# Performance work log

Hardware: AMD Instinct MI355X
Metric: run time of the kernel (lower is better)

Reference implementation:

```python
import jax, jax.numpy as jnp
import numpy as np

# Dims: B=batch, C=n_car, N=n_node, E=embed_dim, H=n_heads
B, C, N, E = 64, 8, 512, 512
H = 8
CLIP = 10.0


def setup_inputs() -> dict:
    key = jax.random.key(0)
    ks = jax.random.split(key, 12)
    s = 1.0 / np.sqrt(E)
    mask = jax.random.bernoulli(ks[10], 0.3, (B, C, 1, N))
    mask = mask.at[..., 0].set(False)  # ensure at least one unmasked node per (b,c)
    return {
        "node_embeddings": jax.random.normal(ks[0], (B, N, E), jnp.float32),
        "graph_embedding": jax.random.normal(ks[1], (B, E), jnp.float32),
        "step_context": jax.random.normal(ks[2], (B, C, 1, E + 2), jnp.float32),
        "mask": mask,
        "Wk1": jax.random.normal(ks[3], (E, E), jnp.float32) * s,
        "Wv": jax.random.normal(ks[4], (E, E), jnp.float32) * s,
        "Wk2": jax.random.normal(ks[5], (E, E), jnp.float32) * s,
        "Wq_fixed": jax.random.normal(ks[6], (E, E), jnp.float32) * s,
        "Wout": jax.random.normal(ks[7], (E, E), jnp.float32) * s,
        "Wq_step": jax.random.normal(ks[8], (E, E + 2), jnp.float32) * s,
        "v": jax.random.uniform(ks[9], (E,), jnp.float32, -s, s),
    }


def reference(node_embeddings, graph_embedding, step_context, mask,
              Wk1, Wv, Wk2, Wq_fixed, Wout, Wq_step, v):
    dh = E // H
    neg = jnp.asarray(-1e9, node_embeddings.dtype)

    # compute_static: projections (torch Linear: x @ W.T). K/V/Q_fixed are
    # broadcast over the car dim instead of materialized via .repeat (same math).
    Q_fixed = (graph_embedding @ Wq_fixed.T)[:, None, None, :]  # [B,1,1,E]
    K1 = node_embeddings @ Wk1.T                                 # [B,N,E]
    V = node_embeddings @ Wv.T                                   # [B,N,E]
    K2 = node_embeddings @ Wk2.T                                 # [B,N,E]

    # compute_dynamic
    Q_step = step_context @ Wq_step.T                            # [B,C,1,E]
    Q1 = Q_fixed + Q_step                                        # [B,C,1,E]

    # MHA (need_W=False): split heads, masked scaled dot-product, merge heads.
    qh = Q1.reshape(B, C, H, dh)                                 # q-len 1 squeezed
    kh = K1.reshape(B, N, H, dh)
    vh = V.reshape(B, N, H, dh)
    scores = jnp.einsum('bchd,bnhd->bchn', qh, kh) * (1.0 / np.sqrt(dh))
    m = mask[:, :, 0, :][:, :, None, :]                          # [B,C,1,N]
    scores = jnp.where(m, neg, scores)
    attn = jax.nn.softmax(scores, axis=-1)
    heads = jnp.einsum('bchn,bnhd->bchd', attn, vh).reshape(B, C, E)
    Q3 = heads @ Wout.T                                          # [B,C,E] (Q2.squeeze(2))

    # Pointer logits (SHA): u = tanh(Q_fixed+Q_step) @ v, repeated over E,
    # dotted with K2 => u_scalar * sum_e K2, then tanh-clipped and masked.
    u_scalar = jnp.einsum('bcqe,e->bcq', jnp.tanh(Q1), v)        # [B,C,1]
    k2sum = K2.sum(-1)                                           # [B,N]
    raw = u_scalar * k2sum[:, None, :]                           # [B,C,N]
    logits = CLIP * jnp.tanh(raw * (1.0 / np.sqrt(E)))
    logits = jnp.where(mask[:, :, 0, :], neg, logits)
    logits = logits.reshape(B, C * N)                            # view(batch, -1)
    return logits, Q3
```

## Files before the change

### kernel.cpp

```cpp
#include <hip/hip_runtime.h>


typedef _Float16 f16x8 __attribute__((ext_vector_type(8)));
typedef float f32x4 __attribute__((ext_vector_type(4)));

__device__ __forceinline__ void async16(const void* g, void* l) {
  __builtin_amdgcn_global_load_lds(
      (const __attribute__((address_space(1))) unsigned int*)g,
      (__attribute__((address_space(3))) unsigned int*)l, 16, 0, 0);
}

__device__ __forceinline__ float fast_tanh(float x) {
  float ax = fabsf(x);
  float t = __expf(-2.f * ax);
  float r = (1.f - t) / (1.f + t);
  return copysignf(r, x);
}

__global__ __launch_bounds__(256) void prep_q1(
    const float* __restrict__ Wk1, const float* __restrict__ Wv,
    const float* __restrict__ Wk2, _Float16* __restrict__ W1h,
    _Float16* __restrict__ W2h, float* __restrict__ colsum,
    const float* __restrict__ ge, const float* __restrict__ sc,
    const float* __restrict__ Wqf, const float* __restrict__ Wqs,
    float* __restrict__ Q1) {
  const int bid = blockIdx.x;
  if (bid < 272) {
    if (bid < 16) {
      const int tx = threadIdx.x & 31, ty = threadIdx.x >> 5;
      const int col = bid * 32 + tx;
      float s = 0.f;
#pragma unroll 4
      for (int e = ty * 64; e < ty * 64 + 64; ++e) s += Wk2[e * 512 + col];
      __shared__ float red[8][32];
      red[ty][tx] = s;
      __syncthreads();
      if (ty == 0) {
        float t = 0.f;
#pragma unroll
        for (int g = 0; g < 8; ++g) t += red[g][tx];
        colsum[col] = t;
      }
    } else {
      const int cb = bid - 16;
      const float* src = (cb < 128) ? Wk1 : Wv;
      _Float16* dst = (cb < 128) ? W1h : W2h;
      const size_t off = (size_t)(cb & 127) * 2048 + threadIdx.x * 8;
      float4 a = *(const float4*)(src + off);
      float4 b = *(const float4*)(src + off + 4);
      union { _Float16 h[8]; uint4 u; } pk;
      pk.h[0] = (_Float16)a.x; pk.h[1] = (_Float16)a.y;
      pk.h[2] = (_Float16)a.z; pk.h[3] = (_Float16)a.w;
      pk.h[4] = (_Float16)b.x; pk.h[5] = (_Float16)b.y;
      pk.h[6] = (_Float16)b.z; pk.h[7] = (_Float16)b.w;
      *(uint4*)(dst + off) = pk.u;
    }
    return;
  }

  const int b2 = bid - 272;
  const int mb = b2 & 7, nb = (b2 >> 3) & 7, ks = b2 >> 6;
  const int tid = threadIdx.x;
  const int lane = tid & 63, wave = tid >> 6;
  const int wm = (wave >> 1) * 32, wn = (wave & 1) * 32;

  __shared__ __align__(16) _Float16 As[64][40];
  __shared__ __align__(16) _Float16 Ws[64][40];

  f32x4 acc[2][2] = {};
  const int qd = (lane >> 4) * 8, rr = lane & 15;

  for (int kt = 0; kt < 9; ++kt) {
    const int kb = ks * 288 + kt * 32;
#pragma unroll
    for (int f0 = 0; f0 < 2; ++f0) {
      int f = tid + f0 * 256;
      int r = f >> 3, c4 = (f & 7) * 4;
      int m = mb * 64 + r;
      int e = nb * 64 + r;
#pragma unroll
      for (int j = 0; j < 4; ++j) {
        int k = kb + c4 + j;
        float a = 0.f, w = 0.f;
        if (k < 512) {
          a = ge[(m >> 3) * 512 + k];
          w = Wqf[(size_t)e * 512 + k];
        } else if (k < 1026) {
          a = sc[(size_t)m * 514 + (k - 512)];
          w = Wqs[(size_t)e * 514 + (k - 512)];
        }
        As[r][c4 + j] = (_Float16)a;
        Ws[r][c4 + j] = (_Float16)w;
      }
    }
    __syncthreads();
    f16x8 af[2], bfr[2];
#pragma unroll
    for (int mi = 0; mi < 2; ++mi) af[mi] = *(const f16x8*)&As[wm + mi * 16 + rr][qd];
#pragma unroll
    for (int ni = 0; ni < 2; ++ni) bfr[ni] = *(const f16x8*)&Ws[wn + ni * 16 + rr][qd];
#pragma unroll
    for (int mi = 0; mi < 2; ++mi)
#pragma unroll
      for (int ni = 0; ni < 2; ++ni)
        acc[mi][ni] =
            __builtin_amdgcn_mfma_f32_16x16x32_f16(af[mi], bfr[ni], acc[mi][ni], 0, 0, 0);
    __syncthreads();
  }

  const int col = lane & 15, rq = (lane >> 4) * 4;
#pragma unroll
  for (int mi = 0; mi < 2; ++mi)
#pragma unroll
    for (int ni = 0; ni < 2; ++ni)
#pragma unroll
      for (int r = 0; r < 4; ++r) {
        int m = mb * 64 + wm + mi * 16 + rq + r;
        int e = nb * 64 + wn + ni * 16 + col;
        atomicAdd(&Q1[(size_t)m * 512 + e], acc[mi][ni][r]);
      }
}

__global__ __launch_bounds__(256, 2) void gemm_kv(
    const float* __restrict__ A, const _Float16* __restrict__ W1,
    const _Float16* __restrict__ W2, const float* __restrict__ colsum,
    _Float16* __restrict__ K1, _Float16* __restrict__ Vt,
    float* __restrict__ k2sum) {
  const int flat = (int)(blockIdx.y * 4 + blockIdx.x);
  const int work = (flat & 7) * 128 + (flat >> 3);
  const int nb = work & 3;
  const int mb = work >> 2;
  const int tid = threadIdx.x, lane = tid & 63, wave = tid >> 6;
  const int wm = (wave >> 1) * 64, wn = (wave & 1) * 64;
  const int row0 = mb * 128, col0 = nb * 128;
  const int b = mb >> 2;

  __shared__ __align__(16) _Float16 Ah[128 * 64];
  __shared__ __align__(16) _Float16 Wb[2][2][128 * 64];

  f32x4 acc1[4][4] = {}, acc2[4][4] = {};
  float k2p[4] = {0.f, 0.f, 0.f, 0.f};
  const int q = lane >> 4, rr = lane & 15;
  const int wlr = lane >> 3, wlc = lane & 7;
  const int cswz = wlc ^ wlr;

  const int ar0 = tid >> 3, ac = tid & 7;
  const float* aptr = A + (size_t)(row0 + ar0) * 512 + ac * 8;
  const int aslot = ac ^ (ar0 & 7);

  float4 areg[4][2];
  float4 cs0, cs1;

  auto issue_a = [&](int kt) {
#pragma unroll
    for (int j = 0; j < 4; ++j) {
      const float* gp = aptr + (size_t)j * 32 * 512 + kt * 64;
      areg[j][0] = *(const float4*)gp;
      areg[j][1] = *(const float4*)(gp + 4);
    }
    if (nb == 0) {
      const float* csp = colsum + kt * 64 + ac * 8;
      cs0 = *(const float4*)csp;
      cs1 = *(const float4*)(csp + 4);
    }
  };
  auto issue_w = [&](int kt, int buf) {
    const int kbase = kt * 64;
#pragma unroll
    for (int j = 0; j < 4; ++j) {
      int r = wave * 32 + j * 8 + wlr;
      int ldsrow = (wave * 32 + j * 8) * 64;
      size_t goff = (size_t)(col0 + r) * 512 + kbase + cswz * 8;
      async16(W1 + goff, &Wb[buf][0][ldsrow]);
      async16(W2 + goff, &Wb[buf][1][ldsrow]);
    }
  };
  auto write_a = [&](int kt) {
#pragma unroll
    for (int j = 0; j < 4; ++j) {
      union { _Float16 h[8]; uint4 u; } pk;
      float4 lo = areg[j][0], hi = areg[j][1];
      pk.h[0] = (_Float16)lo.x; pk.h[1] = (_Float16)lo.y;
      pk.h[2] = (_Float16)lo.z; pk.h[3] = (_Float16)lo.w;
      pk.h[4] = (_Float16)hi.x; pk.h[5] = (_Float16)hi.y;
      pk.h[6] = (_Float16)hi.z; pk.h[7] = (_Float16)hi.w;
      *(uint4*)&Ah[(ar0 + 32 * j) * 64 + aslot * 8] = pk.u;
    }
    if (nb == 0) {
#pragma unroll
      for (int j = 0; j < 4; ++j) {
        float4 lo = areg[j][0], hi = areg[j][1];
        k2p[j] += lo.x * cs0.x + lo.y * cs0.y + lo.z * cs0.z + lo.w * cs0.w +
                  hi.x * cs1.x + hi.y * cs1.y + hi.z * cs1.z + hi.w * cs1.w;
      }
    }
  };

  issue_a(0);
  issue_w(0, 0);
  write_a(0);
  __syncthreads();

  for (int kt = 0; kt < 8; ++kt) {
    const int p = kt & 1;
    if (kt < 7) {
      issue_a(kt + 1);
      issue_w(kt + 1, p ^ 1);
    }
#pragma unroll
    for (int k0 = 0; k0 < 64; k0 += 32) {
      const int cb = (k0 >> 3) + q;
      f16x8 af[4], b1[4], b2[4];
#pragma unroll
      for (int mi = 0; mi < 4; ++mi) {
        int ra = wm + mi * 16 + rr;
        af[mi] = *(const f16x8*)&Ah[ra * 64 + (cb ^ (ra & 7)) * 8];
      }
#pragma unroll
      for (int ni = 0; ni < 4; ++ni) {
        int rw = wn + ni * 16 + rr;
        int slot = cb ^ (rw & 7);
        b1[ni] = *(const f16x8*)&Wb[p][0][rw * 64 + slot * 8];
        b2[ni] = *(const f16x8*)&Wb[p][1][rw * 64 + slot * 8];
      }
      __builtin_amdgcn_s_setprio(1);
#pragma unroll
      for (int mi = 0; mi < 4; ++mi)
#pragma unroll
        for (int ni = 0; ni < 4; ++ni) {
          acc1[mi][ni] =
              __builtin_amdgcn_mfma_f32_16x16x32_f16(af[mi], b1[ni], acc1[mi][ni], 0, 0, 0);
          acc2[mi][ni] =
              __builtin_amdgcn_mfma_f32_16x16x32_f16(af[mi], b2[ni], acc2[mi][ni], 0, 0, 0);
        }
      __builtin_amdgcn_s_setprio(0);
    }
    if (kt < 7) {
      __syncthreads();
      write_a(kt + 1);
      __syncthreads();
    }
  }

  if (nb == 0) {
#pragma unroll
    for (int j = 0; j < 4; ++j) {
      float s = k2p[j];
      s += __shfl_xor(s, 1, 8);
      s += __shfl_xor(s, 2, 8);
      s += __shfl_xor(s, 4, 8);
      if (ac == 0) k2sum[row0 + ar0 + 32 * j] = s;
    }
  }

  const int col = lane & 15, rq = (lane >> 4) * 4;
#pragma unroll
  for (int mi = 0; mi < 4; ++mi)
#pragma unroll
    for (int ni = 0; ni < 4; ++ni)
#pragma unroll
      for (int r = 0; r < 4; ++r) {
        size_t m = row0 + wm + mi * 16 + rq + r;
        size_t e = col0 + wn + ni * 16 + col;
        K1[m * 512 + e] = (_Float16)acc1[mi][ni][r];
      }

  _Float16* Vts = &Wb[0][0][0];
#pragma unroll
  for (int mi = 0; mi < 4; ++mi)
#pragma unroll
    for (int ni = 0; ni < 4; ++ni) {
      int n0 = wm + mi * 16 + rq;
      int el = wn + ni * 16 + col;
      int cn = n0 >> 3, half = (n0 >> 2) & 1;
      int slot = cn ^ (el & 7);
      union { _Float16 h[4]; unsigned long long u; } pk;
#pragma unroll
      for (int r = 0; r < 4; ++r) pk.h[r] = (_Float16)acc2[mi][ni][r];
      *(unsigned long long*)&Vts[el * 128 + slot * 8 + half * 4] = pk.u;
    }
  __syncthreads();
  const int nbase = row0 & 511;
#pragma unroll
  for (int i = 0; i < 8; ++i) {
    int f = tid + i * 256;
    int el = f >> 4, c16 = f & 15;
    int slot = c16 ^ (el & 7);
    uint4 val = *(const uint4*)&Vts[el * 128 + slot * 8];
    *(uint4*)(Vt + (size_t)b * 262144 + (size_t)(col0 + el) * 512 + nbase + c16 * 8) = val;
  }
}

__global__ __launch_bounds__(256) void attn_kernel(
    const float* __restrict__ Q1, const _Float16* __restrict__ K1,
    const _Float16* __restrict__ Vt, const int* __restrict__ mask,
    float* __restrict__ heads) {
  const int bid = blockIdx.x;
  const int b = bid >> 3, h = bid & 7;
  const int tid = threadIdx.x, wave = tid >> 6, lane = tid & 63;
  const int q = lane >> 4, cl = lane & 15;

  __shared__ __align__(16) _Float16 kt[256 * 64];
  __shared__ __align__(16) _Float16 P[16][520];
  __shared__ float red[4][8];

  f16x8 af[2];
  {
    const float* qp = Q1 + (size_t)(b * 8 + (cl & 7)) * 512 + h * 64 + q * 8;
#pragma unroll
    for (int s = 0; s < 2; ++s) {
      float4 l0 = *(const float4*)(qp + s * 32);
      float4 l1 = *(const float4*)(qp + s * 32 + 4);
      af[s][0] = (_Float16)l0.x; af[s][1] = (_Float16)l0.y;
      af[s][2] = (_Float16)l0.z; af[s][3] = (_Float16)l0.w;
      af[s][4] = (_Float16)l1.x; af[s][5] = (_Float16)l1.y;
      af[s][6] = (_Float16)l1.z; af[s][7] = (_Float16)l1.w;
    }
  }

  f32x4 acc[8] = {};
  const _Float16* Kb = K1 + (size_t)b * 262144 + h * 64;
  for (int h2 = 0; h2 < 2; ++h2) {
#pragma unroll
    for (int j = 0; j < 8; ++j) {
      int r = wave * 64 + j * 8 + (lane >> 3);
      int cg = (lane & 7) ^ (r & 7);
      async16(Kb + (size_t)(h2 * 256 + r) * 512 + cg * 8, &kt[(wave * 64 + j * 8) * 64]);
    }
    __syncthreads();
    __builtin_amdgcn_s_setprio(1);
#pragma unroll
    for (int tt = 0; tt < 4; ++tt) {
      int rn = wave * 64 + tt * 16 + cl;
#pragma unroll
      for (int s = 0; s < 2; ++s) {
        int slot = (s * 4 + q) ^ (cl & 7);
        f16x8 bf = *(const f16x8*)&kt[rn * 64 + slot * 8];
        acc[h2 * 4 + tt] =
            __builtin_amdgcn_mfma_f32_16x16x32_f16(af[s], bf, acc[h2 * 4 + tt], 0, 0, 0);
      }
    }
    __builtin_amdgcn_s_setprio(0);
    __syncthreads();
  }

  const _Float16* Vb = Vt + (size_t)b * 262144 + (size_t)h * 64 * 512;
#pragma unroll
  for (int j = 0; j < 8; ++j) {
    int r = wave * 16 + j * 2 + (lane >> 5);
    int cg = (lane & 31) ^ (r & 7);
    async16(Vb + (size_t)r * 512 + cg * 8, &kt[(wave * 16 + j * 2) * 256]);
  }

  float gmax[4], rsum[4];
  if (q < 2) {
    float mx[4] = {-3e38f, -3e38f, -3e38f, -3e38f};
#pragma unroll
    for (int t = 0; t < 8; ++t) {
      int n = (t >> 2) * 256 + wave * 64 + (t & 3) * 16 + cl;
#pragma unroll
      for (int r = 0; r < 4; ++r) {
        int c = q * 4 + r;
        float x = mask[(size_t)(b * 8 + c) * 512 + n] ? -1e9f : acc[t][r] * 0.125f;
        acc[t][r] = x;
        mx[r] = fmaxf(mx[r], x);
      }
    }
#pragma unroll
    for (int off = 1; off < 16; off <<= 1)
#pragma unroll
      for (int r = 0; r < 4; ++r) mx[r] = fmaxf(mx[r], __shfl_xor(mx[r], off, 64));
    if (cl == 0)
#pragma unroll
      for (int r = 0; r < 4; ++r) red[wave][q * 4 + r] = mx[r];
  }
  __syncthreads();
  if (q < 2) {
#pragma unroll
    for (int r = 0; r < 4; ++r) {
      int c = q * 4 + r;
      gmax[r] = fmaxf(fmaxf(red[0][c], red[1][c]), fmaxf(red[2][c], red[3][c]));
    }
  }
  __syncthreads();
  if (q < 2) {
#pragma unroll
    for (int r = 0; r < 4; ++r) rsum[r] = 0.f;
#pragma unroll
    for (int t = 0; t < 8; ++t) {
      int n = (t >> 2) * 256 + wave * 64 + (t & 3) * 16 + cl;
#pragma unroll
      for (int r = 0; r < 4; ++r) {
        float e = __expf(acc[t][r] - gmax[r]);
        rsum[r] += e;
        P[q * 4 + r][n] = (_Float16)e;
      }
    }
#pragma unroll
    for (int off = 1; off < 16; off <<= 1)
#pragma unroll
      for (int r = 0; r < 4; ++r) rsum[r] += __shfl_xor(rsum[r], off, 64);
    if (cl == 0)
#pragma unroll
      for (int r = 0; r < 4; ++r) red[wave][q * 4 + r] = rsum[r];
  }
  __syncthreads();

  f32x4 pacc = {};
  const int rn = wave * 16 + cl;
  __builtin_amdgcn_s_setprio(1);
#pragma unroll
  for (int sl = 0; sl < 8; ++sl) {
    int slot = (sl * 4 + q) ^ (cl & 7);
    f16x8 bf = *(const f16x8*)&kt[rn * 256 + slot * 8];
    f16x8 pa = *(const f16x8*)&P[cl][sl * 32 + q * 8];
    pacc = __builtin_amdgcn_mfma_f32_16x16x32_f16(pa, bf, pacc, 0, 0, 0);
  }
  __builtin_amdgcn_s_setprio(0);
  __syncthreads();
#pragma unroll
  for (int j = 0; j < 8; ++j) {
    int r = wave * 16 + j * 2 + (lane >> 5);
    int cg = (lane & 31) ^ (r & 7);
    async16(Vb + (size_t)r * 512 + 256 + cg * 8, &kt[(wave * 16 + j * 2) * 256]);
  }
  __syncthreads();
  __builtin_amdgcn_s_setprio(1);
#pragma unroll
  for (int sl = 0; sl < 8; ++sl) {
    int slot = (sl * 4 + q) ^ (cl & 7);
    f16x8 bf = *(const f16x8*)&kt[rn * 256 + slot * 8];
    f16x8 pa = *(const f16x8*)&P[cl][256 + sl * 32 + q * 8];
    pacc = __builtin_amdgcn_mfma_f32_16x16x32_f16(pa, bf, pacc, 0, 0, 0);
  }
  __builtin_amdgcn_s_setprio(0);

  if (q < 2) {
#pragma unroll
    for (int r = 0; r < 4; ++r) {
      int c = q * 4 + r;
      float inv = 1.f / (red[0][c] + red[1][c] + red[2][c] + red[3][c]);
      heads[(size_t)(b * 8 + c) * 512 + h * 64 + wave * 16 + cl] = pacc[r] * inv;
    }
  }
}

__global__ __launch_bounds__(256) void out_logits(
    const float* __restrict__ A, const float* __restrict__ W,
    float* __restrict__ C, const float* __restrict__ Q1,
    const float* __restrict__ v, const float* __restrict__ k2s,
    const int* __restrict__ mask, float* __restrict__ out) {
  const int bid = blockIdx.x;
  if (bid < 64) {
    const int mb = bid & 7, nb = bid >> 3;
    const int tid = threadIdx.x;
    const int lane = tid & 63, wave = tid >> 6;
    const int wm = (wave >> 1) * 32, wn = (wave & 1) * 32;

    __shared__ __align__(16) _Float16 As[64][40];
    __shared__ __align__(16) _Float16 Ws[64][40];

    f32x4 acc[2][2] = {};
    const int qd = (lane >> 4) * 8, rr = lane & 15;

    for (int kt = 0; kt < 16; ++kt) {
      const int kb = kt * 32;
#pragma unroll
      for (int f0 = 0; f0 < 2; ++f0) {
        int f = tid + f0 * 256;
        int r = f >> 3, c4 = (f & 7) * 4;
        float4 a = *(const float4*)(A + (size_t)(mb * 64 + r) * 512 + kb + c4);
        float4 w = *(const float4*)(W + (size_t)(nb * 64 + r) * 512 + kb + c4);
        As[r][c4 + 0] = (_Float16)a.x; As[r][c4 + 1] = (_Float16)a.y;
        As[r][c4 + 2] = (_Float16)a.z; As[r][c4 + 3] = (_Float16)a.w;
        Ws[r][c4 + 0] = (_Float16)w.x; Ws[r][c4 + 1] = (_Float16)w.y;
        Ws[r][c4 + 2] = (_Float16)w.z; Ws[r][c4 + 3] = (_Float16)w.w;
      }
      __syncthreads();
      f16x8 af[2], bfr[2];
#pragma unroll
      for (int mi = 0; mi < 2; ++mi) af[mi] = *(const f16x8*)&As[wm + mi * 16 + rr][qd];
#pragma unroll
      for (int ni = 0; ni < 2; ++ni) bfr[ni] = *(const f16x8*)&Ws[wn + ni * 16 + rr][qd];
#pragma unroll
      for (int mi = 0; mi < 2; ++mi)
#pragma unroll
        for (int ni = 0; ni < 2; ++ni)
          acc[mi][ni] =
              __builtin_amdgcn_mfma_f32_16x16x32_f16(af[mi], bfr[ni], acc[mi][ni], 0, 0, 0);
      __syncthreads();
    }

    const int col = lane & 15, rq = (lane >> 4) * 4;
#pragma unroll
    for (int mi = 0; mi < 2; ++mi)
#pragma unroll
      for (int ni = 0; ni < 2; ++ni)
#pragma unroll
        for (int r = 0; r < 4; ++r) {
          int m = mb * 64 + wm + mi * 16 + rq + r;
          int e = nb * 64 + wn + ni * 16 + col;
          C[(size_t)m * 512 + e] = acc[mi][ni][r];
        }
    return;
  }

  const int bc = bid - 64;
  const int b = bc >> 3;
  const int tid = threadIdx.x;
  const int wave = tid >> 6, lane = tid & 63;

  float p = fast_tanh(Q1[(size_t)bc * 512 + tid]) * v[tid] +
            fast_tanh(Q1[(size_t)bc * 512 + tid + 256]) * v[tid + 256];
#pragma unroll
  for (int off = 32; off; off >>= 1) p += __shfl_down(p, off, 64);
  __shared__ float red[4];
  __shared__ float su;
  if (lane == 0) red[wave] = p;
  __syncthreads();
  if (tid == 0) su = red[0] + red[1] + red[2] + red[3];
  __syncthreads();
  const float u = su;

#pragma unroll
  for (int i = 0; i < 2; ++i) {
    int n = tid + i * 256;
    int idx = bc * 512 + n;
    out[idx] = mask[idx] ? -1e9f
                         : 10.f * fast_tanh(u * k2s[b * 512 + n] * 0.04419417382415922f);
  }
}

extern "C" void kernel_launch(void* const* d_in, const int* in_sizes, int n_in,
                              void* d_out, int out_size, void* d_ws, size_t ws_size,
                              hipStream_t stream) {
  const float* ne = (const float*)d_in[0];
  const float* ge = (const float*)d_in[1];
  const float* sc = (const float*)d_in[2];
  const int* mask = (const int*)d_in[3];
  const float* Wk1 = (const float*)d_in[4];
  const float* Wv = (const float*)d_in[5];
  const float* Wk2 = (const float*)d_in[6];
  const float* Wqf = (const float*)d_in[7];
  const float* Wout = (const float*)d_in[8];
  const float* Wqs = (const float*)d_in[9];
  const float* v = (const float*)d_in[10];

  float* logits = (float*)d_out;
  float* q3 = (float*)d_out + 262144;

  char* ws = (char*)d_ws;
  _Float16* K1 = (_Float16*)(ws + 0);
  _Float16* Vt = (_Float16*)(ws + 33554432);
  float* Q1 = (float*)(ws + 67108864);
  float* heads = (float*)(ws + 68157440);
  float* k2sum = (float*)(ws + 69206016);
  float* colsum = (float*)(ws + 69337088);
  _Float16* W1h = (_Float16*)(ws + 69339136);
  _Float16* W2h = (_Float16*)(ws + 69863424);

  hipMemsetAsync(Q1, 0, 1048576, stream);
  prep_q1<<<528, 256, 0, stream>>>(Wk1, Wv, Wk2, W1h, W2h, colsum,
                                   ge, sc, Wqf, Wqs, Q1);
  gemm_kv<<<dim3(4, 256), 256, 0, stream>>>(ne, W1h, W2h, colsum, K1, Vt, k2sum);
  attn_kernel<<<512, 256, 0, stream>>>(Q1, K1, Vt, mask, heads);
  out_logits<<<576, 256, 0, stream>>>(heads, Wout, q3, Q1, v, k2sum, mask, logits);
}
```

Baseline: 209.6 us.

## Double-buffer K/V tiles in attention kernel and split P into halves

The attention kernel now uses two LDS buffers, so the second K half and both V halves are prefetched while the QK MFMAs and softmax run. Before, each load had to wait on the previous compute. P is shrunk to a half-width buffer that is refilled between the two PV passes, and the second half of the exp computation is deferred until after the first PV pass. This adds LDS usage (two 32KB buffers), which may lower occupancy, and changes the barrier schedule.

```diff
diff --git a/kernel.cpp b/kernel.cpp
--- a/kernel.cpp
+++ b/kernel.cpp
@@ -300,8 +300,8 @@
   const int tid = threadIdx.x, wave = tid >> 6, lane = tid & 63;
   const int q = lane >> 4, cl = lane & 15;
 
-  __shared__ __align__(16) _Float16 kt[256 * 64];
-  __shared__ __align__(16) _Float16 P[16][520];
+  __shared__ __align__(16) _Float16 buf[2][256 * 64];
+  __shared__ __align__(16) _Float16 P[16][264];
   __shared__ float red[4][8];
 
   f16x8 af[2];
@@ -318,16 +318,28 @@
     }
   }
 
-  f32x4 acc[8] = {};
   const _Float16* Kb = K1 + (size_t)b * 262144 + h * 64;
-  for (int h2 = 0; h2 < 2; ++h2) {
+  const _Float16* Vb = Vt + (size_t)b * 262144 + (size_t)h * 64 * 512;
+
+  auto stage_K = [&](_Float16* dst, int rbase) {
 #pragma unroll
     for (int j = 0; j < 8; ++j) {
       int r = wave * 64 + j * 8 + (lane >> 3);
       int cg = (lane & 7) ^ (r & 7);
-      async16(Kb + (size_t)(h2 * 256 + r) * 512 + cg * 8, &kt[(wave * 64 + j * 8) * 64]);
-    }
-    __syncthreads();
+      async16(Kb + (size_t)(rbase + r) * 512 + cg * 8, &dst[(wave * 64 + j * 8) * 64]);
+    }
+  };
+  auto stage_V = [&](_Float16* dst, int noff) {
+#pragma unroll
+    for (int j = 0; j < 8; ++j) {
+      int r = wave * 16 + j * 2 + (lane >> 5);
+      int cg = (lane & 31) ^ (r & 7);
+      async16(Vb + (size_t)r * 512 + noff + cg * 8, &dst[(wave * 16 + j * 2) * 256]);
+    }
+  };
+
+  f32x4 acc[8] = {};
+  auto qk_half = [&](const _Float16* src, int h2) {
     __builtin_amdgcn_s_setprio(1);
 #pragma unroll
     for (int tt = 0; tt < 4; ++tt) {
@@ -335,24 +347,25 @@
 #pragma unroll
       for (int s = 0; s < 2; ++s) {
         int slot = (s * 4 + q) ^ (cl & 7);
-        f16x8 bf = *(const f16x8*)&kt[rn * 64 + slot * 8];
+        f16x8 bf = *(const f16x8*)&src[rn * 64 + slot * 8];
         acc[h2 * 4 + tt] =
             __builtin_amdgcn_mfma_f32_16x16x32_f16(af[s], bf, acc[h2 * 4 + tt], 0, 0, 0);
       }
     }
     __builtin_amdgcn_s_setprio(0);
-    __syncthreads();
-  }
-
-  const _Float16* Vb = Vt + (size_t)b * 262144 + (size_t)h * 64 * 512;
-#pragma unroll
-  for (int j = 0; j < 8; ++j) {
-    int r = wave * 16 + j * 2 + (lane >> 5);
-    int cg = (lane & 31) ^ (r & 7);
-    async16(Vb + (size_t)r * 512 + cg * 8, &kt[(wave * 16 + j * 2) * 256]);
-  }
-
-  float gmax[4], rsum[4];
+  };
+
+  stage_K(buf[0], 0);
+  __syncthreads();
+  stage_K(buf[1], 256);
+  qk_half(buf[0], 0);
+  __syncthreads();
+  stage_V(buf[0], 0);
+  qk_half(buf[1], 1);
+  __syncthreads();
+  stage_V(buf[1], 256);
+
+  float gmax[4], rsum[4] = {0.f, 0.f, 0.f, 0.f};
   if (q < 2) {
     float mx[4] = {-3e38f, -3e38f, -3e38f, -3e38f};
 #pragma unroll
@@ -381,28 +394,16 @@
       int c = q * 4 + r;
       gmax[r] = fmaxf(fmaxf(red[0][c], red[1][c]), fmaxf(red[2][c], red[3][c]));
     }
-  }
-  __syncthreads();
-  if (q < 2) {
-#pragma unroll
-    for (int r = 0; r < 4; ++r) rsum[r] = 0.f;
-#pragma unroll
-    for (int t = 0; t < 8; ++t) {
-      int n = (t >> 2) * 256 + wave * 64 + (t & 3) * 16 + cl;
+#pragma unroll
+    for (int t = 0; t < 4; ++t) {
+      int np = wave * 64 + (t & 3) * 16 + cl;
 #pragma unroll
       for (int r = 0; r < 4; ++r) {
         float e = __expf(acc[t][r] - gmax[r]);
         rsum[r] += e;
-        P[q * 4 + r][n] = (_Float16)e;
-      }
-    }
-#pragma unroll
-    for (int off = 1; off < 16; off <<= 1)
-#pragma unroll
-      for (int r = 0; r < 4; ++r) rsum[r] += __shfl_xor(rsum[r], off, 64);
-    if (cl == 0)
-#pragma unroll
-      for (int r = 0; r < 4; ++r) red[wave][q * 4 + r] = rsum[r];
+        P[q * 4 + r][np] = (_Float16)e;
+      }
+    }
   }
   __syncthreads();
 
@@ -412,25 +413,40 @@
 #pragma unroll
   for (int sl = 0; sl < 8; ++sl) {
     int slot = (sl * 4 + q) ^ (cl & 7);
-    f16x8 bf = *(const f16x8*)&kt[rn * 256 + slot * 8];
+    f16x8 bf = *(const f16x8*)&buf[0][rn * 256 + slot * 8];
     f16x8 pa = *(const f16x8*)&P[cl][sl * 32 + q * 8];
     pacc = __builtin_amdgcn_mfma_f32_16x16x32_f16(pa, bf, pacc, 0, 0, 0);
   }
   __builtin_amdgcn_s_setprio(0);
   __syncthreads();
-#pragma unroll
-  for (int j = 0; j < 8; ++j) {
-    int r = wave * 16 + j * 2 + (lane >> 5);
-    int cg = (lane & 31) ^ (r & 7);
-    async16(Vb + (size_t)r * 512 + 256 + cg * 8, &kt[(wave * 16 + j * 2) * 256]);
-  }
-  __syncthreads();
+
+  if (q < 2) {
+#pragma unroll
+    for (int t = 4; t < 8; ++t) {
+      int np = wave * 64 + (t & 3) * 16 + cl;
+#pragma unroll
+      for (int r = 0; r < 4; ++r) {
+        float e = __expf(acc[t][r] - gmax[r]);
+        rsum[r] += e;
+        P[q * 4 + r][np] = (_Float16)e;
+      }
+    }
+#pragma unroll
+    for (int off = 1; off < 16; off <<= 1)
+#pragma unroll
+      for (int r = 0; r < 4; ++r) rsum[r] += __shfl_xor(rsum[r], off, 64);
+    if (cl == 0)
+#pragma unroll
+      for (int r = 0; r < 4; ++r) red[wave][q * 4 + r] = rsum[r];
+  }
+  __syncthreads();
+
   __builtin_amdgcn_s_setprio(1);
 #pragma unroll
   for (int sl = 0; sl < 8; ++sl) {
     int slot = (sl * 4 + q) ^ (cl & 7);
-    f16x8 bf = *(const f16x8*)&kt[rn * 256 + slot * 8];
-    f16x8 pa = *(const f16x8*)&P[cl][256 + sl * 32 + q * 8];
+    f16x8 bf = *(const f16x8*)&buf[1][rn * 256 + slot * 8];
+    f16x8 pa = *(const f16x8*)&P[cl][sl * 32 + q * 8];
     pacc = __builtin_amdgcn_mfma_f32_16x16x32_f16(pa, bf, pacc, 0, 0, 0);
   }
   __builtin_amdgcn_s_setprio(0);
```

Result: no change. 209.1 us (-0.2%).
